# Performance work log

Hardware: AMD Instinct MI355X
Metric: run time of the kernel (lower is better)

Reference implementation:

```python
import jax, jax.numpy as jnp
import numpy as np

E, D_IN, D_HID, D_OUT, B = 8, 128, 256, 128, 65536


def setup_inputs() -> dict:
    key = jax.random.key(0)
    ks = jax.random.split(key, 6)
    s1 = 1.0 / np.sqrt(D_IN)
    s2 = 1.0 / np.sqrt(D_HID)
    return {
        "x": jax.random.normal(ks[0], (B, D_IN), dtype=jnp.float32),
        "weights": jax.random.uniform(ks[1], (B, E), dtype=jnp.float32),
        "W1": jax.random.uniform(ks[2], (E, D_IN, D_HID), jnp.float32, -s1, s1),
        "b1": jax.random.uniform(ks[3], (E, D_HID), jnp.float32, -s1, s1),
        "W2": jax.random.uniform(ks[4], (E, D_HID, D_OUT), jnp.float32, -s2, s2),
        "b2": jax.random.uniform(ks[5], (E, D_OUT), jnp.float32, -s2, s2),
    }


def reference(x, weights, W1, b1, W2, b2):
    # all-experts dense MLP: every expert processes the full batch
    h = jax.nn.relu(jnp.einsum("bi,eih->beh", x, W1) + b1[None])  # [B,E,H]
    y = jnp.einsum("beh,eho->beo", h, W2) + b2[None]              # [B,E,O]
    # weighted combine over experts
    return jnp.einsum("beo,be->bo", y, weights)                   # [B,O]
```

## Files before the change

kernel.cpp:

```cpp
#include <hip/hip_runtime.h>


#define E_    8
#define DIN_  128
#define DH_   256
#define DOUT_ 128
#define BM_   128
#define NCHUNK 32

typedef __attribute__((ext_vector_type(8))) short bf16x8;
typedef __attribute__((ext_vector_type(16))) float f32x16;
typedef __attribute__((ext_vector_type(2))) unsigned int uint2v;

__device__ __forceinline__ unsigned short f2bf(float f) {
  union { float f; unsigned int u; } v; v.f = f;
  unsigned int u = v.u;
  u += 0x7fffu + ((u >> 16) & 1u);
  return (unsigned short)(u >> 16);
}

__device__ __forceinline__ unsigned int cvt_pk_bf16(float lo, float hi) {
  unsigned int r;
  asm("v_cvt_pk_bf16_f32 %0, %1, %2" : "=v"(r) : "v"(lo), "v"(hi));
  return r;
}

__device__ __forceinline__ bf16x8 pack4(unsigned int a, unsigned int b,
                                        unsigned int c, unsigned int d) {
  union { unsigned int u[4]; bf16x8 v; } t;
  t.u[0] = a; t.u[1] = b; t.u[2] = c; t.u[3] = d;
  return t.v;
}

__device__ __forceinline__ void gload_lds16(const void* g, void* l) {
  __builtin_amdgcn_global_load_lds(
      (const __attribute__((address_space(1))) unsigned int*)g,
      (__attribute__((address_space(3))) unsigned int*)l, 16, 0, 0);
}

__global__ __launch_bounds__(256) void transpose_to_bf16(
    const float* __restrict__ in, unsigned short* __restrict__ out,
    int R, int C, int nTR, int nTC)
{
  __shared__ float tile[64][65];
  const int tiles = nTR * nTC;
  const int mat = blockIdx.x / tiles;
  const int tt  = blockIdx.x % tiles;
  const int tr = tt / nTC, tc = tt % nTC;
  const float* src = in + (size_t)mat * R * C;
  unsigned short* dst = out + (size_t)mat * R * C;
  const int tid = threadIdx.x;
  #pragma unroll
  for (int i = 0; i < 16; ++i) {
    int row = i * 4 + (tid >> 6);
    int col = tid & 63;
    tile[row][col] = src[(size_t)(tr * 64 + row) * C + tc * 64 + col];
  }
  __syncthreads();
  #pragma unroll
  for (int i = 0; i < 8; ++i) {
    int c  = i * 8 + (tid >> 5);
    int r0 = (tid & 31) * 2;
    unsigned int pk = (unsigned int)f2bf(tile[r0][c]) |
                      ((unsigned int)f2bf(tile[r0 + 1][c]) << 16);
    *(unsigned int*)(dst + (size_t)(tc * 64 + c) * R + tr * 64 + r0) = pk;
  }
}

__device__ __forceinline__ void stage_chunk(
    const unsigned short* __restrict__ W1t, const unsigned short* __restrict__ W2t,
    unsigned char* buf, int t, int tid, int wv)
{
  const int e = t >> 2, hc = t & 3;
  const unsigned char* w1b =
      (const unsigned char*)(W1t + (size_t)(e * DH_ + hc * 64) * DIN_);
  #pragma unroll
  for (int r = 0; r < 4; ++r) {
    const int o  = (r * 256 + tid) * 16;
    const int c  = o >> 8;
    const int ko = (o & 255) ^ ((c & 7) << 4);
    gload_lds16(w1b + c * 256 + ko, buf + r * 4096 + wv * 1024);
  }
  const unsigned char* w2b = (const unsigned char*)W2t;
  #pragma unroll
  for (int r = 0; r < 4; ++r) {
    const int o  = (r * 256 + tid) * 16;
    const int n  = o >> 7;
    const int co = (o & 127) ^ ((n & 7) << 4);
    gload_lds16(w2b + (size_t)(e * DOUT_ + n) * 512 + hc * 128 + co,
                buf + 16384 + r * 4096 + wv * 1024);
  }
}

__global__ __launch_bounds__(256, 2) void moe_main(
    const float* __restrict__ x, const float* __restrict__ wts,
    const float* __restrict__ b1, const float* __restrict__ b2,
    const unsigned short* __restrict__ W1t, const unsigned short* __restrict__ W2t,
    float* __restrict__ out)
{
  __shared__ __align__(16) unsigned char Wbuf[2][32768];

  const int tid  = threadIdx.x;
  const int lane = tid & 63;
  const int wv   = tid >> 6;
  const int l32  = lane & 31;
  const int hi   = lane >> 5;
  const int swz  = (l32 & 7) << 4;
  const long bm  = (long)blockIdx.x * BM_;
  const int m    = wv * 32 + l32;

  stage_chunk(W1t, W2t, Wbuf[0], 0, tid, wv);

  float wreg[8];
  {
    float4 a = *(const float4*)(wts + (bm + m) * E_);
    float4 b = *(const float4*)(wts + (bm + m) * E_ + 4);
    wreg[0] = a.x; wreg[1] = a.y; wreg[2] = a.z; wreg[3] = a.w;
    wreg[4] = b.x; wreg[5] = b.y; wreg[6] = b.z; wreg[7] = b.w;
  }

  bf16x8 xf[8];
  #pragma unroll
  for (int ks = 0; ks < 8; ++ks) {
    const float* xr = x + (bm + m) * DIN_ + ks * 16 + hi * 8;
    float4 a = *(const float4*)xr;
    float4 b = *(const float4*)(xr + 4);
    xf[ks] = pack4(cvt_pk_bf16(a.x, a.y), cvt_pk_bf16(a.z, a.w),
                   cvt_pk_bf16(b.x, b.y), cvt_pk_bf16(b.z, b.w));
  }

  f32x16 oacc[4];
  #pragma unroll
  for (int nf = 0; nf < 4; ++nf) oacc[nf] = 0.0f;

  for (int t = 0; t < NCHUNK; ++t) {
    const int e = t >> 2, hc = t & 3;
    const unsigned char* Wc = Wbuf[t & 1];
    __syncthreads();

    float bb[2][16];
    #pragma unroll
    for (int cf = 0; cf < 2; ++cf)
      #pragma unroll
      for (int g = 0; g < 4; ++g) {
        float4 b = *(const float4*)(b1 + e * DH_ + hc * 64 + cf * 32 + g * 8 + hi * 4);
        bb[cf][4 * g + 0] = b.x; bb[cf][4 * g + 1] = b.y;
        bb[cf][4 * g + 2] = b.z; bb[cf][4 * g + 3] = b.w;
      }

    if (t + 1 < NCHUNK) stage_chunk(W1t, W2t, Wbuf[(t + 1) & 1], t + 1, tid, wv);

    f32x16 hacc[2];
    hacc[0] = 0.0f; hacc[1] = 0.0f;
    #pragma unroll
    for (int ks = 0; ks < 8; ++ks) {
      const int kb = ks * 32 + hi * 16;
      #pragma unroll
      for (int cf = 0; cf < 2; ++cf) {
        bf16x8 a = *(const bf16x8*)(Wc + (cf * 32 + l32) * 256 + (kb ^ swz));
        hacc[cf] = __builtin_amdgcn_mfma_f32_32x32x16_bf16(a, xf[ks], hacc[cf], 0, 0, 0);
      }
    }

    const float w = wreg[e];
    bf16x8 hfr[4];
    #pragma unroll
    for (int cf = 0; cf < 2; ++cf) {
      unsigned int u[8];
      #pragma unroll
      for (int p = 0; p < 8; ++p) {
        float h0 = fmaxf(hacc[cf][2 * p]     + bb[cf][2 * p],     0.0f) * w;
        float h1 = fmaxf(hacc[cf][2 * p + 1] + bb[cf][2 * p + 1], 0.0f) * w;
        u[p] = cvt_pk_bf16(h0, h1);
      }
      uint2v s02 = __builtin_amdgcn_permlane32_swap(u[0], u[2], false, false);
      uint2v s13 = __builtin_amdgcn_permlane32_swap(u[1], u[3], false, false);
      uint2v s46 = __builtin_amdgcn_permlane32_swap(u[4], u[6], false, false);
      uint2v s57 = __builtin_amdgcn_permlane32_swap(u[5], u[7], false, false);
      hfr[2 * cf]     = pack4(s02[0], s13[0], s02[1], s13[1]);
      hfr[2 * cf + 1] = pack4(s46[0], s57[0], s46[1], s57[1]);
    }

    #pragma unroll
    for (int ks = 0; ks < 4; ++ks) {
      const int cb = ks * 32 + hi * 16;
      #pragma unroll
      for (int nf = 0; nf < 4; ++nf) {
        bf16x8 b = *(const bf16x8*)(Wc + 16384 + (nf * 32 + l32) * 128 + (cb ^ swz));
        oacc[nf] = __builtin_amdgcn_mfma_f32_32x32x16_bf16(hfr[ks], b, oacc[nf], 0, 0, 0);
      }
    }
  }

  const unsigned int z = 0;
  bf16x8 wfrag = pack4(hi ? z : cvt_pk_bf16(wreg[0], wreg[1]),
                       hi ? z : cvt_pk_bf16(wreg[2], wreg[3]),
                       hi ? z : cvt_pk_bf16(wreg[4], wreg[5]),
                       hi ? z : cvt_pk_bf16(wreg[6], wreg[7]));
  #pragma unroll
  for (int nf = 0; nf < 4; ++nf) {
    const float* bp = b2 + nf * 32 + l32;
    bf16x8 bfrag = pack4(
        hi ? z : cvt_pk_bf16(bp[0 * DOUT_], bp[1 * DOUT_]),
        hi ? z : cvt_pk_bf16(bp[2 * DOUT_], bp[3 * DOUT_]),
        hi ? z : cvt_pk_bf16(bp[4 * DOUT_], bp[5 * DOUT_]),
        hi ? z : cvt_pk_bf16(bp[6 * DOUT_], bp[7 * DOUT_]));
    oacc[nf] = __builtin_amdgcn_mfma_f32_32x32x16_bf16(wfrag, bfrag, oacc[nf], 0, 0, 0);
  }

  #pragma unroll
  for (int nf = 0; nf < 4; ++nf) {
    #pragma unroll
    for (int r = 0; r < 16; ++r) {
      const int mloc = (r & 3) + 8 * (r >> 2) + 4 * hi;
      out[(bm + wv * 32 + mloc) * DOUT_ + nf * 32 + l32] = oacc[nf][r];
    }
  }
}

extern "C" void kernel_launch(void* const* d_in, const int* in_sizes, int n_in,
                              void* d_out, int out_size, void* d_ws, size_t ws_size,
                              hipStream_t stream) {
  const float* x   = (const float*)d_in[0];
  const float* wts = (const float*)d_in[1];
  const float* W1  = (const float*)d_in[2];
  const float* b1  = (const float*)d_in[3];
  const float* W2  = (const float*)d_in[4];
  const float* b2  = (const float*)d_in[5];
  float* out = (float*)d_out;

  unsigned short* W1t = (unsigned short*)d_ws;
  unsigned short* W2t = W1t + (size_t)E_ * DH_ * DIN_;

  transpose_to_bf16<<<64, 256, 0, stream>>>(W1, W1t, 128, 256, 2, 4);
  transpose_to_bf16<<<64, 256, 0, stream>>>(W2, W2t, 256, 128, 4, 2);

  moe_main<<<65536 / BM_, 256, 0, stream>>>(x, wts, b1, b2, W1t, W2t, out);
}
```

Measured before the change: 93.82 us.

## Pack per-chunk weight records and double per-wave M tile with 2-wave blocks

Replaces the two transpose kernels with one prep kernel that writes contiguous, pre-swizzled bf16 records per chunk (W1 slice, W2 slice, b1 bias), so staging becomes a flat copy of 17 16-byte loads per thread. The main kernel now uses 128-thread blocks where each wave computes 64 rows (two M tiles), so every LDS weight fragment feeds two MFMAs. The b1 bias is folded into the accumulator through an extra MFMA against a ones vector, and the loop is unrolled by two over the double buffer. Occupancy changes to one block of two waves per launch bound with more registers per wave, which may hurt latency hiding.

```diff
diff --git a/kernel.cpp b/kernel.cpp
--- a/kernel.cpp
+++ b/kernel.cpp
@@ -7,6 +7,7 @@
 #define DOUT_ 128
 #define BM_   128
 #define NCHUNK 32
+#define RECSZ 34816
 
 typedef __attribute__((ext_vector_type(8))) short bf16x8;
 typedef __attribute__((ext_vector_type(16))) float f32x16;
@@ -38,67 +39,69 @@
       (__attribute__((address_space(3))) unsigned int*)l, 16, 0, 0);
 }
 
-__global__ __launch_bounds__(256) void transpose_to_bf16(
-    const float* __restrict__ in, unsigned short* __restrict__ out,
-    int R, int C, int nTR, int nTC)
+__global__ __launch_bounds__(256) void prep_pack(
+    const float* __restrict__ W1, const float* __restrict__ W2,
+    const float* __restrict__ b1, unsigned char* __restrict__ Wall)
 {
-  __shared__ float tile[64][65];
-  const int tiles = nTR * nTC;
-  const int mat = blockIdx.x / tiles;
-  const int tt  = blockIdx.x % tiles;
-  const int tr = tt / nTC, tc = tt % nTC;
-  const float* src = in + (size_t)mat * R * C;
-  unsigned short* dst = out + (size_t)mat * R * C;
+  __shared__ float T[8192];
+  const int bid = blockIdx.x;
+  const int t = bid >> 1, region = bid & 1;
+  const int e = t >> 2, hc = t & 3;
   const int tid = threadIdx.x;
-  #pragma unroll
-  for (int i = 0; i < 16; ++i) {
-    int row = i * 4 + (tid >> 6);
-    int col = tid & 63;
-    tile[row][col] = src[(size_t)(tr * 64 + row) * C + tc * 64 + col];
-  }
-  __syncthreads();
-  #pragma unroll
-  for (int i = 0; i < 8; ++i) {
-    int c  = i * 8 + (tid >> 5);
-    int r0 = (tid & 31) * 2;
-    unsigned int pk = (unsigned int)f2bf(tile[r0][c]) |
-                      ((unsigned int)f2bf(tile[r0 + 1][c]) << 16);
-    *(unsigned int*)(dst + (size_t)(tc * 64 + c) * R + tr * 64 + r0) = pk;
-  }
-}
-
-__device__ __forceinline__ void stage_chunk(
-    const unsigned short* __restrict__ W1t, const unsigned short* __restrict__ W2t,
-    unsigned char* buf, int t, int tid, int wv)
-{
-  const int e = t >> 2, hc = t & 3;
-  const unsigned char* w1b =
-      (const unsigned char*)(W1t + (size_t)(e * DH_ + hc * 64) * DIN_);
-  #pragma unroll
-  for (int r = 0; r < 4; ++r) {
-    const int o  = (r * 256 + tid) * 16;
-    const int c  = o >> 8;
-    const int ko = (o & 255) ^ ((c & 7) << 4);
-    gload_lds16(w1b + c * 256 + ko, buf + r * 4096 + wv * 1024);
-  }
-  const unsigned char* w2b = (const unsigned char*)W2t;
-  #pragma unroll
-  for (int r = 0; r < 4; ++r) {
-    const int o  = (r * 256 + tid) * 16;
-    const int n  = o >> 7;
-    const int co = (o & 127) ^ ((n & 7) << 4);
-    gload_lds16(w2b + (size_t)(e * DOUT_ + n) * 512 + hc * 128 + co,
-                buf + 16384 + r * 4096 + wv * 1024);
-  }
-}
-
-__global__ __launch_bounds__(256, 2) void moe_main(
+  unsigned char* rec = Wall + (size_t)t * RECSZ;
+
+  if (region == 0) {
+    #pragma unroll
+    for (int i = 0; i < 32; ++i) {
+      int idx = i * 256 + tid;
+      int k = idx >> 6, c = idx & 63;
+      T[idx] = W1[((size_t)(e * DIN_ + k)) * DH_ + hc * 64 + c];
+    }
+    __syncthreads();
+    #pragma unroll
+    for (int j = 0; j < 16; ++j) {
+      int widx = j * 256 + tid;
+      int c = widx >> 6, uw = (widx & 63) * 4;
+      int up = uw ^ ((c & 7) << 4);
+      int k0 = up >> 1;
+      unsigned int val = (unsigned int)f2bf(T[k0 * 64 + c]) |
+                         ((unsigned int)f2bf(T[(k0 + 1) * 64 + c]) << 16);
+      *(unsigned int*)(rec + c * 256 + uw) = val;
+    }
+    if (tid < 64) {
+      *(unsigned int*)(rec + 32768 + tid * 32) =
+          (unsigned int)f2bf(b1[e * DH_ + hc * 64 + tid]);
+      #pragma unroll
+      for (int p = 1; p < 8; ++p)
+        *(unsigned int*)(rec + 32768 + tid * 32 + p * 4) = 0u;
+    }
+  } else {
+    #pragma unroll
+    for (int i = 0; i < 32; ++i) {
+      int idx = i * 256 + tid;
+      int h = idx >> 7, n = idx & 127;
+      T[idx] = W2[((size_t)(e * DH_ + hc * 64 + h)) * DOUT_ + n];
+    }
+    __syncthreads();
+    #pragma unroll
+    for (int j = 0; j < 16; ++j) {
+      int widx = j * 256 + tid;
+      int n = widx >> 5, uw = (widx & 31) * 4;
+      int up = uw ^ ((n & 7) << 4);
+      int h0 = up >> 1;
+      unsigned int val = (unsigned int)f2bf(T[h0 * 128 + n]) |
+                         ((unsigned int)f2bf(T[(h0 + 1) * 128 + n]) << 16);
+      *(unsigned int*)(rec + 16384 + n * 128 + uw) = val;
+    }
+  }
+}
+
+__global__ __launch_bounds__(128, 1) void moe_main(
     const float* __restrict__ x, const float* __restrict__ wts,
-    const float* __restrict__ b1, const float* __restrict__ b2,
-    const unsigned short* __restrict__ W1t, const unsigned short* __restrict__ W2t,
+    const float* __restrict__ b2, const unsigned char* __restrict__ Wall,
     float* __restrict__ out)
 {
-  __shared__ __align__(16) unsigned char Wbuf[2][32768];
+  __shared__ __align__(16) unsigned char L[2][RECSZ];
 
   const int tid  = threadIdx.x;
   const int lane = tid & 63;
@@ -107,96 +110,136 @@
   const int hi   = lane >> 5;
   const int swz  = (l32 & 7) << 4;
   const long bm  = (long)blockIdx.x * BM_;
-  const int m    = wv * 32 + l32;
-
-  stage_chunk(W1t, W2t, Wbuf[0], 0, tid, wv);
-
-  float wreg[8];
+  const long row0 = bm + wv * 64 + l32;
+
+  auto stage = [&](int t, unsigned char* dst) {
+    const unsigned char* src = Wall + (size_t)t * RECSZ;
+    #pragma unroll
+    for (int r = 0; r < 17; ++r)
+      gload_lds16(src + (r * 128 + tid) * 16, dst + r * 2048 + wv * 1024);
+  };
+
+  stage(0, L[0]);
+
+  int p1o[8], p2o[4];
+  #pragma unroll
+  for (int ks = 0; ks < 8; ++ks)
+    p1o[ks] = l32 * 256 + ((ks * 32 + hi * 16) ^ swz);
+  #pragma unroll
+  for (int k2 = 0; k2 < 4; ++k2)
+    p2o[k2] = 16384 + l32 * 128 + ((k2 * 32 + hi * 16) ^ swz);
+  const int bo = 32768 + l32 * 32 + hi * 16;
+
+  const bf16x8 ones = pack4(hi ? 0u : 0x3F80u, 0u, 0u, 0u);
+
+  bf16x8 xf[2][8];
+  #pragma unroll
+  for (int mt = 0; mt < 2; ++mt) {
+    const float* xr0 = x + (row0 + mt * 32) * DIN_;
+    #pragma unroll
+    for (int ks = 0; ks < 8; ++ks) {
+      const float* xr = xr0 + ks * 16 + hi * 8;
+      float4 a = *(const float4*)xr;
+      float4 b = *(const float4*)(xr + 4);
+      xf[mt][ks] = pack4(cvt_pk_bf16(a.x, a.y), cvt_pk_bf16(a.z, a.w),
+                         cvt_pk_bf16(b.x, b.y), cvt_pk_bf16(b.z, b.w));
+    }
+  }
+
+  const float* wp0 = wts + row0 * E_;
+  const float* wp1 = wts + (row0 + 32) * E_;
+
+  f32x16 oacc[2][4];
+  #pragma unroll
+  for (int mt = 0; mt < 2; ++mt)
+    #pragma unroll
+    for (int nf = 0; nf < 4; ++nf) oacc[mt][nf] = 0.0f;
+
+  auto chunk = [&](const unsigned char* Lb, int t) {
+    const int e = t >> 2;
+    const float wA = wp0[e], wB = wp1[e];
+
+    f32x16 h[2][2];
+    h[0][0] = 0.0f; h[0][1] = 0.0f; h[1][0] = 0.0f; h[1][1] = 0.0f;
+    #pragma unroll
+    for (int ks = 0; ks < 8; ++ks) {
+      bf16x8 a0 = *(const bf16x8*)(Lb + p1o[ks]);
+      bf16x8 a1 = *(const bf16x8*)(Lb + p1o[ks] + 8192);
+      h[0][0] = __builtin_amdgcn_mfma_f32_32x32x16_bf16(a0, xf[0][ks], h[0][0], 0, 0, 0);
+      h[0][1] = __builtin_amdgcn_mfma_f32_32x32x16_bf16(a0, xf[1][ks], h[0][1], 0, 0, 0);
+      h[1][0] = __builtin_amdgcn_mfma_f32_32x32x16_bf16(a1, xf[0][ks], h[1][0], 0, 0, 0);
+      h[1][1] = __builtin_amdgcn_mfma_f32_32x32x16_bf16(a1, xf[1][ks], h[1][1], 0, 0, 0);
+    }
+    {
+      bf16x8 bf0 = *(const bf16x8*)(Lb + bo);
+      bf16x8 bf1 = *(const bf16x8*)(Lb + bo + 1024);
+      h[0][0] = __builtin_amdgcn_mfma_f32_32x32x16_bf16(bf0, ones, h[0][0], 0, 0, 0);
+      h[0][1] = __builtin_amdgcn_mfma_f32_32x32x16_bf16(bf0, ones, h[0][1], 0, 0, 0);
+      h[1][0] = __builtin_amdgcn_mfma_f32_32x32x16_bf16(bf1, ones, h[1][0], 0, 0, 0);
+      h[1][1] = __builtin_amdgcn_mfma_f32_32x32x16_bf16(bf1, ones, h[1][1], 0, 0, 0);
+    }
+
+    bf16x8 hfr[2][4];
+    #pragma unroll
+    for (int mt = 0; mt < 2; ++mt) {
+      const float w = mt ? wB : wA;
+      #pragma unroll
+      for (int cf = 0; cf < 2; ++cf) {
+        unsigned int u[8];
+        #pragma unroll
+        for (int p = 0; p < 8; ++p) {
+          float h0 = fmaxf(h[cf][mt][2 * p],     0.0f) * w;
+          float h1 = fmaxf(h[cf][mt][2 * p + 1], 0.0f) * w;
+          u[p] = cvt_pk_bf16(h0, h1);
+        }
+        uint2v s02 = __builtin_amdgcn_permlane32_swap(u[0], u[2], false, false);
+        uint2v s13 = __builtin_amdgcn_permlane32_swap(u[1], u[3], false, false);
+        uint2v s46 = __builtin_amdgcn_permlane32_swap(u[4], u[6], false, false);
+        uint2v s57 = __builtin_amdgcn_permlane32_swap(u[5], u[7], false, false);
+        hfr[mt][2 * cf]     = pack4(s02[0], s13[0], s02[1], s13[1]);
+        hfr[mt][2 * cf + 1] = pack4(s46[0], s57[0], s46[1], s57[1]);
+      }
+    }
+
+    #pragma unroll
+    for (int k2 = 0; k2 < 4; ++k2) {
+      #pragma unroll
+      for (int nf = 0; nf < 4; ++nf) {
+        bf16x8 b = *(const bf16x8*)(Lb + p2o[k2] + nf * 4096);
+        oacc[0][nf] = __builtin_amdgcn_mfma_f32_32x32x16_bf16(hfr[0][k2], b, oacc[0][nf], 0, 0, 0);
+        oacc[1][nf] = __builtin_amdgcn_mfma_f32_32x32x16_bf16(hfr[1][k2], b, oacc[1][nf], 0, 0, 0);
+      }
+    }
+  };
+
+  for (int tt = 0; tt < NCHUNK; tt += 2) {
+    __syncthreads();
+    if (tt + 1 < NCHUNK) stage(tt + 1, L[1]);
+    chunk(L[0], tt);
+    __syncthreads();
+    if (tt + 2 < NCHUNK) stage(tt + 2, L[0]);
+    chunk(L[1], tt + 1);
+  }
+
+  const unsigned int z = 0;
+  float wv0[8], wv1[8];
   {
-    float4 a = *(const float4*)(wts + (bm + m) * E_);
-    float4 b = *(const float4*)(wts + (bm + m) * E_ + 4);
-    wreg[0] = a.x; wreg[1] = a.y; wreg[2] = a.z; wreg[3] = a.w;
-    wreg[4] = b.x; wreg[5] = b.y; wreg[6] = b.z; wreg[7] = b.w;
-  }
-
-  bf16x8 xf[8];
-  #pragma unroll
-  for (int ks = 0; ks < 8; ++ks) {
-    const float* xr = x + (bm + m) * DIN_ + ks * 16 + hi * 8;
-    float4 a = *(const float4*)xr;
-    float4 b = *(const float4*)(xr + 4);
-    xf[ks] = pack4(cvt_pk_bf16(a.x, a.y), cvt_pk_bf16(a.z, a.w),
-                   cvt_pk_bf16(b.x, b.y), cvt_pk_bf16(b.z, b.w));
-  }
-
-  f32x16 oacc[4];
-  #pragma unroll
-  for (int nf = 0; nf < 4; ++nf) oacc[nf] = 0.0f;
-
-  for (int t = 0; t < NCHUNK; ++t) {
-    const int e = t >> 2, hc = t & 3;
-    const unsigned char* Wc = Wbuf[t & 1];
-    __syncthreads();
-
-    float bb[2][16];
-    #pragma unroll
-    for (int cf = 0; cf < 2; ++cf)
-      #pragma unroll
-      for (int g = 0; g < 4; ++g) {
-        float4 b = *(const float4*)(b1 + e * DH_ + hc * 64 + cf * 32 + g * 8 + hi * 4);
-        bb[cf][4 * g + 0] = b.x; bb[cf][4 * g + 1] = b.y;
-        bb[cf][4 * g + 2] = b.z; bb[cf][4 * g + 3] = b.w;
-      }
-
-    if (t + 1 < NCHUNK) stage_chunk(W1t, W2t, Wbuf[(t + 1) & 1], t + 1, tid, wv);
-
-    f32x16 hacc[2];
-    hacc[0] = 0.0f; hacc[1] = 0.0f;
-    #pragma unroll
-    for (int ks = 0; ks < 8; ++ks) {
-      const int kb = ks * 32 + hi * 16;
-      #pragma unroll
-      for (int cf = 0; cf < 2; ++cf) {
-        bf16x8 a = *(const bf16x8*)(Wc + (cf * 32 + l32) * 256 + (kb ^ swz));
-        hacc[cf] = __builtin_amdgcn_mfma_f32_32x32x16_bf16(a, xf[ks], hacc[cf], 0, 0, 0);
-      }
-    }
-
-    const float w = wreg[e];
-    bf16x8 hfr[4];
-    #pragma unroll
-    for (int cf = 0; cf < 2; ++cf) {
-      unsigned int u[8];
-      #pragma unroll
-      for (int p = 0; p < 8; ++p) {
-        float h0 = fmaxf(hacc[cf][2 * p]     + bb[cf][2 * p],     0.0f) * w;
-        float h1 = fmaxf(hacc[cf][2 * p + 1] + bb[cf][2 * p + 1], 0.0f) * w;
-        u[p] = cvt_pk_bf16(h0, h1);
-      }
-      uint2v s02 = __builtin_amdgcn_permlane32_swap(u[0], u[2], false, false);
-      uint2v s13 = __builtin_amdgcn_permlane32_swap(u[1], u[3], false, false);
-      uint2v s46 = __builtin_amdgcn_permlane32_swap(u[4], u[6], false, false);
-      uint2v s57 = __builtin_amdgcn_permlane32_swap(u[5], u[7], false, false);
-      hfr[2 * cf]     = pack4(s02[0], s13[0], s02[1], s13[1]);
-      hfr[2 * cf + 1] = pack4(s46[0], s57[0], s46[1], s57[1]);
-    }
-
-    #pragma unroll
-    for (int ks = 0; ks < 4; ++ks) {
-      const int cb = ks * 32 + hi * 16;
-      #pragma unroll
-      for (int nf = 0; nf < 4; ++nf) {
-        bf16x8 b = *(const bf16x8*)(Wc + 16384 + (nf * 32 + l32) * 128 + (cb ^ swz));
-        oacc[nf] = __builtin_amdgcn_mfma_f32_32x32x16_bf16(hfr[ks], b, oacc[nf], 0, 0, 0);
-      }
-    }
-  }
-
-  const unsigned int z = 0;
-  bf16x8 wfrag = pack4(hi ? z : cvt_pk_bf16(wreg[0], wreg[1]),
-                       hi ? z : cvt_pk_bf16(wreg[2], wreg[3]),
-                       hi ? z : cvt_pk_bf16(wreg[4], wreg[5]),
-                       hi ? z : cvt_pk_bf16(wreg[6], wreg[7]));
+    float4 a = *(const float4*)wp0; float4 b = *(const float4*)(wp0 + 4);
+    wv0[0]=a.x; wv0[1]=a.y; wv0[2]=a.z; wv0[3]=a.w;
+    wv0[4]=b.x; wv0[5]=b.y; wv0[6]=b.z; wv0[7]=b.w;
+    float4 c = *(const float4*)wp1; float4 d = *(const float4*)(wp1 + 4);
+    wv1[0]=c.x; wv1[1]=c.y; wv1[2]=c.z; wv1[3]=c.w;
+    wv1[4]=d.x; wv1[5]=d.y; wv1[6]=d.z; wv1[7]=d.w;
+  }
+  bf16x8 wfrag[2];
+  wfrag[0] = pack4(hi ? z : cvt_pk_bf16(wv0[0], wv0[1]),
+                   hi ? z : cvt_pk_bf16(wv0[2], wv0[3]),
+                   hi ? z : cvt_pk_bf16(wv0[4], wv0[5]),
+                   hi ? z : cvt_pk_bf16(wv0[6], wv0[7]));
+  wfrag[1] = pack4(hi ? z : cvt_pk_bf16(wv1[0], wv1[1]),
+                   hi ? z : cvt_pk_bf16(wv1[2], wv1[3]),
+                   hi ? z : cvt_pk_bf16(wv1[4], wv1[5]),
+                   hi ? z : cvt_pk_bf16(wv1[6], wv1[7]));
   #pragma unroll
   for (int nf = 0; nf < 4; ++nf) {
     const float* bp = b2 + nf * 32 + l32;
@@ -205,15 +248,20 @@
         hi ? z : cvt_pk_bf16(bp[2 * DOUT_], bp[3 * DOUT_]),
         hi ? z : cvt_pk_bf16(bp[4 * DOUT_], bp[5 * DOUT_]),
         hi ? z : cvt_pk_bf16(bp[6 * DOUT_], bp[7 * DOUT_]));
-    oacc[nf] = __builtin_amdgcn_mfma_f32_32x32x16_bf16(wfrag, bfrag, oacc[nf], 0, 0, 0);
-  }
-
-  #pragma unroll
-  for (int nf = 0; nf < 4; ++nf) {
-    #pragma unroll
-    for (int r = 0; r < 16; ++r) {
-      const int mloc = (r & 3) + 8 * (r >> 2) + 4 * hi;
-      out[(bm + wv * 32 + mloc) * DOUT_ + nf * 32 + l32] = oacc[nf][r];
+    oacc[0][nf] = __builtin_amdgcn_mfma_f32_32x32x16_bf16(wfrag[0], bfrag, oacc[0][nf], 0, 0, 0);
+    oacc[1][nf] = __builtin_amdgcn_mfma_f32_32x32x16_bf16(wfrag[1], bfrag, oacc[1][nf], 0, 0, 0);
+  }
+
+  #pragma unroll
+  for (int mt = 0; mt < 2; ++mt) {
+    #pragma unroll
+    for (int nf = 0; nf < 4; ++nf) {
+      #pragma unroll
+      for (int r = 0; r < 16; ++r) {
+        const int mloc = (r & 3) + 8 * (r >> 2) + 4 * hi;
+        out[(bm + wv * 64 + mt * 32 + mloc) * DOUT_ + nf * 32 + l32] =
+            oacc[mt][nf][r];
+      }
     }
   }
 }
@@ -229,11 +277,8 @@
   const float* b2  = (const float*)d_in[5];
   float* out = (float*)d_out;
 
-  unsigned short* W1t = (unsigned short*)d_ws;
-  unsigned short* W2t = W1t + (size_t)E_ * DH_ * DIN_;
-
-  transpose_to_bf16<<<64, 256, 0, stream>>>(W1, W1t, 128, 256, 2, 4);
-  transpose_to_bf16<<<64, 256, 0, stream>>>(W2, W2t, 256, 128, 4, 2);
-
-  moe_main<<<65536 / BM_, 256, 0, stream>>>(x, wts, b1, b2, W1t, W2t, out);
-}
+  unsigned char* Wall = (unsigned char*)d_ws;
+
+  prep_pack<<<64, 256, 0, stream>>>(W1, W2, b1, Wall);
+  moe_main<<<65536 / BM_, 128, 0, stream>>>(x, wts, b2, Wall, out);
+}
```

After: 95.21 us. About the same (+1.5%).
